# Kernel tuning notes

Hardware: AMD Instinct MI355X
Metric: run time of the kernel (lower is better)

The kernel has to match this reference:

```python
import jax, jax.numpy as jnp
import numpy as np
from jax import lax

D_MODEL = 128
D_INNER = 256   # expand * d_model
D_STATE = 16
D_CONV = 4
DT_RANK = 8     # ceil(d_model / 16)
IN_CH = 64
SCALE = 0.02


def setup_inputs() -> dict:
    key = jax.random.key(0)
    ks = jax.random.split(key, 16)
    r = lambda k, s: jax.random.normal(k, s, dtype=jnp.float32)
    return {
        "x": r(ks[0], (4, IN_CH, 128, 128)),
        "conv_w": r(ks[1], (D_MODEL, IN_CH, 3, 3)) * SCALE,
        "conv_b": r(ks[2], (D_MODEL,)) * SCALE,
        "bn_g": jnp.ones((D_MODEL,), jnp.float32),
        "bn_b": jnp.zeros((D_MODEL,), jnp.float32),
        "bn_mean": r(ks[3], (D_MODEL,)) * SCALE,
        "bn_var": jax.random.uniform(ks[4], (D_MODEL,), jnp.float32) + 0.5,
        "in_w": r(ks[5], (2 * D_INNER, D_MODEL)) * SCALE,
        "conv1d_w": r(ks[6], (D_INNER, 1, D_CONV)) * SCALE,
        "conv1d_b": r(ks[7], (D_INNER,)) * SCALE,
        "xproj_w": r(ks[8], (DT_RANK + 2 * D_STATE, D_INNER)) * SCALE,
        "dtproj_w": r(ks[9], (D_INNER, DT_RANK)) * SCALE,
        "dtproj_b": r(ks[10], (D_INNER,)) * SCALE,
        "A_log": r(ks[11], (D_INNER, D_STATE)) * 0.5,
        "Dp": r(ks[12], (D_INNER,)) * SCALE,
        "out_w": r(ks[13], (D_MODEL, D_INNER)) * SCALE,
    }


def _mamba(u, in_w, conv1d_w, conv1d_b, xproj_w, dtproj_w, dtproj_b, A_log, Dp, out_w):
    # u: [B, L, d_model]
    xz = jnp.einsum("bld,ed->ble", u, in_w)          # [B, L, 2*d_inner]
    x_in, z = jnp.split(xz, 2, axis=-1)
    # depthwise causal conv1d over L
    xc = lax.conv_general_dilated(
        x_in.transpose(0, 2, 1), conv1d_w, (1,), [(D_CONV - 1, 0)],
        dimension_numbers=("NCL", "OIL", "NCL"), feature_group_count=D_INNER,
    ) + conv1d_b[None, :, None]
    x_in = jax.nn.silu(xc).transpose(0, 2, 1)         # [B, L, d_inner]

    x_dbl = jnp.einsum("bld,ed->ble", x_in, xproj_w)  # [B, L, dt_rank+2*d_state]
    dt, Bm, Cm = jnp.split(x_dbl, [DT_RANK, DT_RANK + D_STATE], axis=-1)
    delta = jax.nn.softplus(jnp.einsum("blr,dr->bld", dt, dtproj_w) + dtproj_b)

    A = -jnp.exp(A_log)                               # [d_inner, d_state]
    deltaA = jnp.exp(jnp.einsum("bld,dn->bldn", delta, A))        # [B,L,d,n]
    deltaBu = jnp.einsum("bld,bln,bld->bldn", delta, Bm, x_in)    # [B,L,d,n]

    def step(h, inp):
        dA, dBu, c = inp                              # [B,d,n],[B,d,n],[B,n]
        h = dA * h + dBu
        y = jnp.einsum("bdn,bn->bd", h, c)
        return h, y

    Bsz, L = u.shape[0], u.shape[1]
    h0 = jnp.zeros((Bsz, D_INNER, D_STATE), u.dtype)
    _, ys = lax.scan(step, h0, (deltaA.transpose(1, 0, 2, 3),
                                deltaBu.transpose(1, 0, 2, 3),
                                Cm.transpose(1, 0, 2)))
    y = ys.transpose(1, 0, 2) + x_in * Dp             # [B, L, d_inner]
    y = y * jax.nn.silu(z)
    return jnp.einsum("bld,ed->ble", y, out_w)        # [B, L, d_model]


def reference(x, conv_w, conv_b, bn_g, bn_b, bn_mean, bn_var, in_w, conv1d_w,
              conv1d_b, xproj_w, dtproj_w, dtproj_b, A_log, Dp, out_w):
    # downsample: conv3x3 stride2 + BN(eval) + exact GELU
    y = lax.conv_general_dilated(x, conv_w, (2, 2), [(1, 1), (1, 1)],
                                 dimension_numbers=("NCHW", "OIHW", "NCHW"))
    y = y + conv_b[None, :, None, None]
    inv = bn_g / jnp.sqrt(bn_var + 1e-5)
    y = (y - bn_mean[None, :, None, None]) * inv[None, :, None, None] + bn_b[None, :, None, None]
    y = jax.nn.gelu(y, approximate=False)             # [B, C, H, W]

    B, C, H, W = y.shape
    u = y.reshape(B, C, H * W).transpose(0, 2, 1)     # [B, L, C]
    out = _mamba(u, in_w, conv1d_w, conv1d_b, xproj_w, dtproj_w, dtproj_b,
                 A_log, Dp, out_w)
    out = out.transpose(0, 2, 1).reshape(B, C, H, W)
    return y + out
```

## Files before the change

### kernel.cpp

```cpp
#include <hip/hip_runtime.h>
#include <math.h>

#define NB 4
#define LTOK 4096
#define DM 128
#define DI 256
#define NCH 256
#define TCH 16
#define GSZ 16
#define NG  16

#define OFF_A2     0u
#define OFF_BIAS2  73728u
#define OFF_YDSR   84096u
#define OFF_XPRE   2181248u
#define OFF_S0     4278400u
#define OFF_Z      6375552u
#define OFF_DELTA  10569856u
#define OFF_S1     12667008u
#define OFF_BC     14764160u
#define OFF_DSUM   15288448u
#define OFF_GS     15550592u
#define OFF_GD     15812736u
#define OFF_XT     15829120u
#define OFF_WBF    17926272u
#define OFF_WCMP   17963136u
#define OFF_YDSBF  18004096u
#define OFF_DPREF  18004096u
#define OFF_INWBF  19052672u
#define OFF_OUTWBF 19085440u

#define DEV __device__ __forceinline__
#define L2E 1.4426950408889634f

typedef short bh8 __attribute__((ext_vector_type(8)));
typedef float f4v __attribute__((ext_vector_type(4)));

DEV float fast_silu(float v) {
  return v * __builtin_amdgcn_rcpf(1.f + __expf(-v));
}

DEV unsigned short f2bf(float f) {
  unsigned int u = __float_as_uint(f);
  u = (u + 0x7FFFu + ((u >> 16) & 1u)) >> 16;
  return (unsigned short)u;
}

DEV float bf2f(unsigned short us) {
  return __uint_as_float((unsigned int)us << 16);
}

__global__ __launch_bounds__(256) void k0_prep(
    const float* __restrict__ conv_w, const float* __restrict__ conv_b,
    const float* __restrict__ bn_g, const float* __restrict__ bn_b,
    const float* __restrict__ bn_mean, const float* __restrict__ bn_var,
    const float* __restrict__ xproj_w, const float* __restrict__ A_log,
    const float* __restrict__ dtw, const float* __restrict__ in_w,
    const float* __restrict__ out_w, float* __restrict__ ws) {
  int i = blockIdx.x * 256 + threadIdx.x;
  if (i < 73728) {
    int ci = i & 63; int tap = (i >> 6) % 9; int co = i / 576;
    float inv = bn_g[co] * rsqrtf(bn_var[co] + 1e-5f);
    ((unsigned short*)(ws + OFF_WBF))[i] = f2bf(conv_w[co * 576 + ci * 9 + tap] * inv);
  } else if (i < 73856) {
    int co = i - 73728;
    float inv = bn_g[co] * rsqrtf(bn_var[co] + 1e-5f);
    ws[OFF_BIAS2 + co] = (conv_b[co] - bn_mean[co]) * inv + bn_b[co];
  } else if (i < 77952) {
    int j = i - 73856;
    ws[OFF_A2 + j] = -__expf(A_log[j]) * L2E;
  } else if (i < 159872) {
    int j = i - 77952;
    int n = j >> 8, k = j & 255;
    float v = 0.f;
    if (n < 256) {
#pragma unroll
      for (int r = 0; r < 8; ++r)
        v = fmaf(dtw[n * 8 + r], xproj_w[r * 256 + k], v);
    } else if (n < 288) {
      v = xproj_w[(8 + n - 256) * 256 + k];
    }
    ((unsigned short*)(ws + OFF_WCMP))[j] = f2bf(v);
  } else if (i < 225408) {
    int j = i - 159872;
    ((unsigned short*)(ws + OFF_INWBF))[j] = f2bf(in_w[j]);
  } else if (i < 258176) {
    int j = i - 225408;
    ((unsigned short*)(ws + OFF_OUTWBF))[j] = f2bf(out_w[j]);
  }
}

__global__ __launch_bounds__(256) void k0b_transpose(
    const float* __restrict__ x, unsigned short* __restrict__ xt) {
  __shared__ float t[64][65];
  const int tid = threadIdx.x;
  const int ixh = blockIdx.x & 1;
  const int iy = (blockIdx.x >> 1) & 127;
  const int b = blockIdx.x >> 8;
  {
    const int ixl = tid & 63, cw = tid >> 6;
#pragma unroll 4
    for (int i = 0; i < 16; ++i) {
      int ci = cw * 16 + i;
      t[ci][ixl] = x[(((size_t)(b * 64 + ci) * 128) + iy) * 128 + ixh * 64 + ixl];
    }
  }
  __syncthreads();
  {
    const int cil = tid & 63, iw = tid >> 6;
    unsigned short* dst = xt + (((size_t)(b * 128 + iy) * 128) + ixh * 64) * 64;
#pragma unroll 4
    for (int i = 0; i < 16; ++i) {
      int ix = iw * 16 + i;
      dst[ix * 64 + cil] = f2bf(t[cil][ix]);
    }
  }
}

__global__ __launch_bounds__(256) void k1_conv_mfma(
    const unsigned short* __restrict__ xt, const unsigned short* __restrict__ wbf,
    const float* __restrict__ bias2, unsigned short* __restrict__ ydsr,
    unsigned short* __restrict__ ydsbf) {
  __shared__ unsigned short ldt[64][66];
  const int tid = threadIdx.x;
  const int lane = tid & 63;
  const int w = tid >> 6;
  const int col = lane & 15, quad = lane >> 4;
  const int cohalf = blockIdx.x & 1;
  const int oy = (blockIdx.x >> 1) & 63;
  const int b = blockIdx.x >> 7;
  const int co0 = cohalf * 64 + (w & 1) * 32;
  const int tok0 = (w >> 1) * 32;
  const int iy0 = 2 * oy - 1;
  const bh8 bzero = {};
  f4v acc[2][2];
#pragma unroll
  for (int mt = 0; mt < 2; ++mt)
#pragma unroll
    for (int nt = 0; nt < 2; ++nt) acc[mt][nt] = (f4v){0.f, 0.f, 0.f, 0.f};

  const unsigned short* ap0 = wbf + (size_t)(co0 + col) * 576;
  const unsigned short* ap1 = wbf + (size_t)(co0 + 16 + col) * 576;

  for (int tap = 0; tap < 9; ++tap) {
    const int kh = tap / 3, kw = tap - kh * 3;
    const int iy = iy0 + kh;
    const int ix0 = 2 * (tok0 + col) - 1 + kw;
    const int ix1 = ix0 + 32;
    const unsigned short* xrow = xt + (long)(b * 128 + iy) * 8192;
    const bool ok0 = (iy >= 0) && (ix0 >= 0);
    const bool ok1 = (iy >= 0);
#pragma unroll
    for (int kc = 0; kc < 2; ++kc) {
      const int cib = kc * 32 + quad * 8;
      bh8 a0 = *(const bh8*)&ap0[tap * 64 + cib];
      bh8 a1 = *(const bh8*)&ap1[tap * 64 + cib];
      bh8 b0 = *(const bh8*)&xrow[(long)ix0 * 64 + cib];
      bh8 b1 = *(const bh8*)&xrow[(long)ix1 * 64 + cib];
      if (!ok0) b0 = bzero;
      if (!ok1) b1 = bzero;
      acc[0][0] = __builtin_amdgcn_mfma_f32_16x16x32_bf16(a0, b0, acc[0][0], 0, 0, 0);
      acc[1][0] = __builtin_amdgcn_mfma_f32_16x16x32_bf16(a1, b0, acc[1][0], 0, 0, 0);
      acc[0][1] = __builtin_amdgcn_mfma_f32_16x16x32_bf16(a0, b1, acc[0][1], 0, 0, 0);
      acc[1][1] = __builtin_amdgcn_mfma_f32_16x16x32_bf16(a1, b1, acc[1][1], 0, 0, 0);
    }
  }
#pragma unroll
  for (int mt = 0; mt < 2; ++mt)
#pragma unroll
    for (int nt = 0; nt < 2; ++nt) {
      const int tok = tok0 + nt * 16 + col;
#pragma unroll
      for (int r = 0; r < 4; ++r) {
        const int co = co0 + mt * 16 + quad * 4 + r;
        float v = acc[mt][nt][r] + bias2[co];
        float g = 0.5f * v * (1.f + erff(v * 0.70710678118f));
        unsigned short gb = f2bf(g);
        ydsr[(((size_t)(b * 128 + co) * 64) + oy) * 64 + tok] = gb;
        ldt[tok][(w & 1) * 32 + mt * 16 + quad * 4 + r] = gb;
      }
    }
  __syncthreads();
  {
    const int tok = tid >> 2, cg = (tid & 3) * 16;
    unsigned short* dst =
        ydsbf + ((size_t)(b * 4096 + oy * 64 + tok)) * 128 + cohalf * 64 + cg;
#pragma unroll
    for (int j = 0; j < 8; ++j)
      ((unsigned int*)dst)[j] = *(const unsigned int*)&ldt[tok][cg + 2 * j];
  }
}

__global__ __launch_bounds__(256) void k2_mfma(
    const unsigned short* __restrict__ ydsbf, const unsigned short* __restrict__ inwbf,
    unsigned short* __restrict__ xpre, unsigned short* __restrict__ z) {
  const int tid = threadIdx.x;
  const int lane = tid & 63;
  const int w = tid >> 6;
  const int col = lane & 15, quad = lane >> 4;
  const int tt = blockIdx.x & 255, b = blockIdx.x >> 8;
  const int t0 = tt * 16;
  bh8 afrag[4];
  {
    const unsigned short* arow = ydsbf + (size_t)(b * 4096 + t0 + col) * 128 + quad * 8;
#pragma unroll
    for (int kb = 0; kb < 4; ++kb) afrag[kb] = *(const bh8*)&arow[kb * 32];
  }
  f4v acc[8];
#pragma unroll
  for (int j = 0; j < 8; ++j) acc[j] = (f4v){0.f, 0.f, 0.f, 0.f};
  const int nt0 = w * 8;
  const unsigned short* wb = inwbf + (size_t)(nt0 * 16 + col) * 128 + quad * 8;
#pragma unroll
  for (int kb = 0; kb < 4; ++kb) {
#pragma unroll
    for (int j = 0; j < 8; ++j) {
      bh8 bfrag = *(const bh8*)&wb[(size_t)j * 2048 + kb * 32];
      acc[j] = __builtin_amdgcn_mfma_f32_16x16x32_bf16(afrag[kb], bfrag, acc[j], 0, 0, 0);
    }
  }
#pragma unroll
  for (int j = 0; j < 8; ++j) {
    const int e = (nt0 + j) * 16 + col;
#pragma unroll
    for (int r = 0; r < 4; ++r) {
      const int t = t0 + quad * 4 + r;
      if (e < 256) xpre[((size_t)(b * 4096 + t)) * 256 + e] = f2bf(acc[j][r]);
      else z[((size_t)(b * 4096 + t)) * 256 + e - 256] = f2bf(acc[j][r]);
    }
  }
}

__global__ __launch_bounds__(256) void k45_mfma(
    const unsigned short* __restrict__ wcomp, const float* __restrict__ dtb,
    const unsigned short* __restrict__ xpre, const float* __restrict__ cw1,
    const float* __restrict__ cb1, const float* __restrict__ a2tab,
    unsigned short* __restrict__ xinbf, unsigned short* __restrict__ delta,
    float* __restrict__ bc, float* __restrict__ dsum,
    float* __restrict__ S0, float* __restrict__ S1) {
  __shared__ unsigned short ld_xin[16][264];
  __shared__ unsigned short ld_delta[16][264];
  __shared__ float ld_bc[16][33];
  const int tid = threadIdx.x;
  const int lane = tid & 63;
  const int w = tid >> 6;
  const int col = lane & 15, quad = lane >> 4;
  const int tt = blockIdx.x & 255, b = blockIdx.x >> 8;
  const int t0 = tt * 16;

  {
    const int d = tid;
    float4 w4 = *(const float4*)&cw1[d * 4];
    float bias = cb1[d];
    float xw[19];
#pragma unroll
    for (int i = 0; i < 19; ++i) {
      int t = t0 - 3 + i;
      xw[i] = (t >= 0) ? bf2f(xpre[((size_t)(b * 4096 + t)) * 256 + d]) : 0.f;
    }
    unsigned short* dst = xinbf + ((size_t)(b * 4096 + t0)) * 256 + d;
#pragma unroll
    for (int i = 0; i < 16; ++i) {
      float o = bias + w4.x * xw[i] + w4.y * xw[i + 1] + w4.z * xw[i + 2] +
                w4.w * xw[i + 3];
      unsigned short us = f2bf(fast_silu(o));
      ld_xin[i][d] = us;
      dst[(size_t)i * 256] = us;
    }
  }
  __syncthreads();

  {
    bh8 afrag[8];
#pragma unroll
    for (int kb = 0; kb < 8; ++kb)
      afrag[kb] = *(const bh8*)&ld_xin[col][quad * 8 + kb * 32];
    f4v acc[5];
#pragma unroll
    for (int j = 0; j < 5; ++j) acc[j] = (f4v){0.f, 0.f, 0.f, 0.f};

    const int nt0 = w * 5;
    const unsigned short* wb = wcomp + (size_t)(nt0 * 16 + col) * 256 + quad * 8;
#pragma unroll
    for (int kb = 0; kb < 8; ++kb) {
#pragma unroll
      for (int j = 0; j < 5; ++j) {
        bh8 bfrag = *(const bh8*)&wb[(size_t)j * 4096 + kb * 32];
        acc[j] = __builtin_amdgcn_mfma_f32_16x16x32_bf16(afrag[kb], bfrag, acc[j], 0, 0, 0);
      }
    }
#pragma unroll
    for (int j = 0; j < 5; ++j) {
      const int n = (nt0 + j) * 16 + col;
      if (n < 256) {
        float bias = dtb[n];
#pragma unroll
        for (int r = 0; r < 4; ++r) {
          float s = acc[j][r] + bias;
          float dl = fmaxf(s, 0.f) + __logf(1.f + __expf(-fabsf(s)));
          ld_delta[quad * 4 + r][n] = f2bf(dl);
        }
      } else if (n < 288) {
#pragma unroll
        for (int r = 0; r < 4; ++r) ld_bc[quad * 4 + r][n - 256] = acc[j][r];
      }
    }
  }
  __syncthreads();

  {
    const int d = tid;
    float A2[16];
#pragma unroll
    for (int j = 0; j < 4; ++j) {
      float4 a = *(const float4*)&a2tab[d * 16 + j * 4];
      A2[4 * j + 0] = a.x; A2[4 * j + 1] = a.y;
      A2[4 * j + 2] = a.z; A2[4 * j + 3] = a.w;
    }
    float h[16];
#pragma unroll
    for (int n = 0; n < 16; ++n) h[n] = 0.f;
    float ds = 0.f;
#pragma unroll 4
    for (int i = 0; i < TCH; ++i) {
      float dl = bf2f(ld_delta[i][d]);
      float xv = bf2f(ld_xin[i][d]);
      ds += dl;
      float dlx = dl * xv;
#pragma unroll
      for (int n = 0; n < 16; ++n)
        h[n] = fmaf(exp2f(dl * A2[n]), h[n], dlx * ld_bc[i][n]);
    }
    dsum[((size_t)b * NCH + tt) * 256 + d] = ds;
    float* S = (b & 2) ? (S1 + (size_t)(b & 1) * 1048576)
                       : (S0 + (size_t)(b & 1) * 1048576);
    const size_t sbase = ((size_t)tt * 16) * 256 + d;
#pragma unroll
    for (int n = 0; n < 16; ++n) S[sbase + (size_t)n * 256] = h[n];
  }

#pragma unroll
  for (int it = 0; it < 4; ++it) {
    int idx = it * 256 + tid;
    int row = idx >> 6, d4 = (idx & 63) * 4;
    unsigned long long pk = *(const unsigned long long*)&ld_delta[row][d4];
    *(unsigned long long*)&delta[((size_t)(b * 4096 + t0 + row)) * 256 + d4] = pk;
  }
  if (tid < 128) {
    int row = tid >> 3, q = (tid & 7) * 4;
    float4 v = make_float4(ld_bc[row][q], ld_bc[row][q + 1],
                           ld_bc[row][q + 2], ld_bc[row][q + 3]);
    *(float4*)&bc[((size_t)(b * 4096 + t0 + row)) * 32 + q] = v;
  }
}

__global__ __launch_bounds__(256) void k5b1_group(
    float* __restrict__ S0, float* __restrict__ S1,
    const float* __restrict__ dsum, const float* __restrict__ a2tab,
    float* __restrict__ Gs, float* __restrict__ Gd,
    float* __restrict__ dpref) {
  const int d = threadIdx.x;
  const int n = blockIdx.x & 15, g = (blockIdx.x >> 4) & (NG - 1),
            b = blockIdx.x >> 8;
  float* S = (b & 2) ? (S1 + (size_t)(b & 1) * 1048576)
                     : (S0 + (size_t)(b & 1) * 1048576);
  const float A2 = a2tab[d * 16 + n];
  const size_t s0 = ((size_t)(g * GSZ) * 16 + n) * 256 + d;
  const size_t d0 = ((size_t)b * NCH + g * GSZ) * 256 + d;
  float sv[GSZ], dv[GSZ];
#pragma unroll
  for (int k = 0; k < GSZ; ++k) {
    sv[k] = S[s0 + (size_t)k * 4096];
    dv[k] = dsum[d0 + (size_t)k * 256];
  }
  float h = 0.f, cum = 0.f;
#pragma unroll
  for (int k = 0; k < GSZ; ++k) {
    S[s0 + (size_t)k * 4096] = h;
    if (n == 0) dpref[d0 + (size_t)k * 256] = cum;
    h = fmaf(exp2f(A2 * dv[k]), h, sv[k]);
    cum += dv[k];
  }
  Gs[((size_t)(b * NG + g) * 16 + n) * 256 + d] = h;
  if (n == 0) Gd[((size_t)b * NG + g) * 256 + d] = cum;
}

__global__ __launch_bounds__(256) void k5b2_groupscan(
    float* __restrict__ Gs, const float* __restrict__ Gd,
    const float* __restrict__ a2tab) {
  const int d = threadIdx.x;
  const int n = blockIdx.x & 15, b = blockIdx.x >> 4;
  const float A2 = a2tab[d * 16 + n];
  float sv[NG], dv[NG];
  const size_t g0 = ((size_t)(b * NG) * 16 + n) * 256 + d;
  const size_t gd0 = (size_t)b * NG * 256 + d;
#pragma unroll
  for (int g = 0; g < NG; ++g) {
    sv[g] = Gs[g0 + (size_t)g * 4096];
    dv[g] = Gd[gd0 + (size_t)g * 256];
  }
  float h = 0.f;
#pragma unroll
  for (int g = 0; g < NG; ++g) {
    Gs[g0 + (size_t)g * 4096] = h;
    h = fmaf(exp2f(A2 * dv[g]), h, sv[g]);
  }
}

__global__ __launch_bounds__(256) void k56_fused(
    const unsigned short* __restrict__ xinbf, const float* __restrict__ bc,
    const unsigned short* __restrict__ delta, const unsigned short* __restrict__ z,
    const float* __restrict__ a2tab, const float* __restrict__ Dp,
    const float* __restrict__ dpref, const float* __restrict__ Gs,
    const float* __restrict__ S0, const float* __restrict__ S1,
    const unsigned short* __restrict__ outwbf, const unsigned short* __restrict__ ydsr,
    float* __restrict__ out) {
  __shared__ __align__(16) float bct[TCH * 32];
  __shared__ __align__(16) unsigned short ld_y[16][264];
  __shared__ float ldo[16][132];
  const int tid = threadIdx.x;
  const int d = tid;
  const int c = blockIdx.x & (NCH - 1), b = blockIdx.x >> 8;
  const int t0 = c * TCH;
  {
    const float* src = bc + (size_t)(b * 4096 + t0) * 32;
    for (int i = tid; i < TCH * 32; i += 256) bct[i] = src[i];
  }
  float A2[16];
#pragma unroll
  for (int j = 0; j < 4; ++j) {
    float4 a = *(const float4*)&a2tab[d * 16 + j * 4];
    A2[4 * j + 0] = a.x; A2[4 * j + 1] = a.y;
    A2[4 * j + 2] = a.z; A2[4 * j + 3] = a.w;
  }
  const float Dpd = Dp[d];
  const int g = c >> 4;
  const float dp0 = dpref[((size_t)b * NCH + c) * 256 + d];
  const float* S = (b & 2) ? (S1 + (size_t)(b & 1) * 1048576)
                           : (S0 + (size_t)(b & 1) * 1048576);
  const size_t sbase = ((size_t)c * 16) * 256 + d;
  const size_t gbase = ((size_t)(b * NG + g) * 16) * 256 + d;
  float h[16];
#pragma unroll
  for (int n = 0; n < 16; ++n) {
    float gi = Gs[gbase + (size_t)n * 256];
    float hl = S[sbase + (size_t)n * 256];
    h[n] = fmaf(exp2f(A2[n] * dp0), gi, hl);
  }
  const size_t base = (size_t)(b * 4096 + t0) * 256 + d;
  const unsigned short* pd = delta + base;
  const unsigned short* px = xinbf + base;
  const unsigned short* pz = z + base;
  __syncthreads();
#pragma unroll 4
  for (int i = 0; i < TCH; ++i) {
    float dl = bf2f(pd[(size_t)i * 256]);
    float xv = bf2f(px[(size_t)i * 256]);
    float zv = bf2f(pz[(size_t)i * 256]);
    float dlx = dl * xv;
    const float* r = &bct[i * 32];
    float4 B0 = *(const float4*)&r[0];
    float4 B1 = *(const float4*)&r[4];
    float4 B2 = *(const float4*)&r[8];
    float4 B3 = *(const float4*)&r[12];
    float4 C0 = *(const float4*)&r[16];
    float4 C1 = *(const float4*)&r[20];
    float4 C2 = *(const float4*)&r[24];
    float4 C3 = *(const float4*)&r[28];
    float Bv[16] = {B0.x, B0.y, B0.z, B0.w, B1.x, B1.y, B1.z, B1.w,
                    B2.x, B2.y, B2.z, B2.w, B3.x, B3.y, B3.z, B3.w};
    float Cv[16] = {C0.x, C0.y, C0.z, C0.w, C1.x, C1.y, C1.z, C1.w,
                    C2.x, C2.y, C2.z, C2.w, C3.x, C3.y, C3.z, C3.w};
    float y = 0.f;
#pragma unroll
    for (int n = 0; n < 16; ++n) {
      h[n] = fmaf(exp2f(dl * A2[n]), h[n], dlx * Bv[n]);
      y = fmaf(h[n], Cv[n], y);
    }
    ld_y[i][d] = f2bf((y + xv * Dpd) * fast_silu(zv));
  }
  __syncthreads();

  const int lane = tid & 63;
  const int w = tid >> 6;
  const int col = lane & 15, quad = lane >> 4;
  const int oy = t0 >> 6, ox0 = t0 & 63;
  bh8 afrag[8];
#pragma unroll
  for (int kb = 0; kb < 8; ++kb)
    afrag[kb] = *(const bh8*)&ld_y[col][quad * 8 + kb * 32];
  f4v acc[2];
#pragma unroll
  for (int j = 0; j < 2; ++j) acc[j] = (f4v){0.f, 0.f, 0.f, 0.f};
  const int nt0 = w * 2;
  const unsigned short* wb = outwbf + (size_t)(nt0 * 16 + col) * 256 + quad * 8;
#pragma unroll
  for (int kb = 0; kb < 8; ++kb) {
#pragma unroll
    for (int j = 0; j < 2; ++j) {
      bh8 bfrag = *(const bh8*)&wb[(size_t)j * 4096 + kb * 32];
      acc[j] = __builtin_amdgcn_mfma_f32_16x16x32_bf16(afrag[kb], bfrag, acc[j], 0, 0, 0);
    }
  }
#pragma unroll
  for (int j = 0; j < 2; ++j)
#pragma unroll
    for (int r = 0; r < 4; ++r)
      ldo[quad * 4 + r][(nt0 + j) * 16 + col] = acc[j][r];
  __syncthreads();
  {
    const int cc = tid >> 1, half = tid & 1;
    size_t obase = (((size_t)(b * 128 + cc) * 64) + oy) * 64 + ox0 + half * 8;
    const unsigned short* rp = ydsr + obase;
    const int m0 = half * 8;
    float4 o0 = make_float4(ldo[m0 + 0][cc] + bf2f(rp[0]), ldo[m0 + 1][cc] + bf2f(rp[1]),
                            ldo[m0 + 2][cc] + bf2f(rp[2]), ldo[m0 + 3][cc] + bf2f(rp[3]));
    float4 o1 = make_float4(ldo[m0 + 4][cc] + bf2f(rp[4]), ldo[m0 + 5][cc] + bf2f(rp[5]),
                            ldo[m0 + 6][cc] + bf2f(rp[6]), ldo[m0 + 7][cc] + bf2f(rp[7]));
    *(float4*)&out[obase] = o0;
    *(float4*)&out[obase + 4] = o1;
  }
}

extern "C" void kernel_launch(void* const* d_in, const int* in_sizes, int n_in,
                              void* d_out, int out_size, void* d_ws, size_t ws_size,
                              hipStream_t stream) {
  (void)in_sizes; (void)n_in; (void)out_size; (void)ws_size;
  const float* x        = (const float*)d_in[0];
  const float* conv_w   = (const float*)d_in[1];
  const float* conv_b   = (const float*)d_in[2];
  const float* bn_g     = (const float*)d_in[3];
  const float* bn_b     = (const float*)d_in[4];
  const float* bn_mean  = (const float*)d_in[5];
  const float* bn_var   = (const float*)d_in[6];
  const float* in_w     = (const float*)d_in[7];
  const float* conv1d_w = (const float*)d_in[8];
  const float* conv1d_b = (const float*)d_in[9];
  const float* xproj_w  = (const float*)d_in[10];
  const float* dtproj_w = (const float*)d_in[11];
  const float* dtproj_b = (const float*)d_in[12];
  const float* A_log    = (const float*)d_in[13];
  const float* Dp       = (const float*)d_in[14];
  const float* out_w    = (const float*)d_in[15];
  float* ws = (float*)d_ws;
  float* out = (float*)d_out;

  k0_prep<<<1009, 256, 0, stream>>>(conv_w, conv_b, bn_g, bn_b, bn_mean, bn_var,
                                    xproj_w, A_log, dtproj_w, in_w, out_w, ws);
  k0b_transpose<<<1024, 256, 0, stream>>>(x, (unsigned short*)(ws + OFF_XT));
  k1_conv_mfma<<<512, 256, 0, stream>>>((const unsigned short*)(ws + OFF_XT),
                                        (const unsigned short*)(ws + OFF_WBF),
                                        ws + OFF_BIAS2,
                                        (unsigned short*)(ws + OFF_YDSR),
                                        (unsigned short*)(ws + OFF_YDSBF));
  k2_mfma<<<1024, 256, 0, stream>>>((const unsigned short*)(ws + OFF_YDSBF),
                                    (const unsigned short*)(ws + OFF_INWBF),
                                    (unsigned short*)(ws + OFF_XPRE),
                                    (unsigned short*)(ws + OFF_Z));
  k45_mfma<<<1024, 256, 0, stream>>>((const unsigned short*)(ws + OFF_WCMP),
                                     dtproj_b,
                                     (const unsigned short*)(ws + OFF_XPRE),
                                     conv1d_w, conv1d_b, ws + OFF_A2,
                                     (unsigned short*)(ws + OFF_XT),
                                     (unsigned short*)(ws + OFF_DELTA),
                                     ws + OFF_BC, ws + OFF_DSUM,
                                     ws + OFF_S0, ws + OFF_S1);
  k5b1_group<<<1024, 256, 0, stream>>>(ws + OFF_S0, ws + OFF_S1, ws + OFF_DSUM,
                                       ws + OFF_A2, ws + OFF_GS, ws + OFF_GD,
                                       ws + OFF_DPREF);
  k5b2_groupscan<<<64, 256, 0, stream>>>(ws + OFF_GS, ws + OFF_GD, ws + OFF_A2);
  k56_fused<<<1024, 256, 0, stream>>>((const unsigned short*)(ws + OFF_XT),
                                      ws + OFF_BC,
                                      (const unsigned short*)(ws + OFF_DELTA),
                                      (const unsigned short*)(ws + OFF_Z),
                                      ws + OFF_A2, Dp, ws + OFF_DPREF,
                                      ws + OFF_GS, ws + OFF_S0, ws + OFF_S1,
                                      (const unsigned short*)(ws + OFF_OUTWBF),
                                      (const unsigned short*)(ws + OFF_YDSR), out);
}
```

Baseline: 215.7 us.

## Fuse conv with in-projection, merge prep with transpose, and inline group scan

Merges the weight-prep and input-transpose kernels into one launch using a block-index split. Fuses the 3x3 conv+GELU kernel with the in-projection GEMM so each block keeps its 64 tokens x 128 channels tile in swizzled LDS. This removes the ydsbf round trip through global memory. Drops the separate group-scan kernel; each k56 block now recomputes the prefix over earlier groups from Gs/Gd. That adds redundant serial work (up to 15 steps) and fewer, larger conv blocks (256 blocks of 512 threads).

```diff
diff --git a/kernel.cpp b/kernel.cpp
--- a/kernel.cpp
+++ b/kernel.cpp
@@ -25,7 +25,6 @@
 #define OFF_XT     15829120u
 #define OFF_WBF    17926272u
 #define OFF_WCMP   17963136u
-#define OFF_YDSBF  18004096u
 #define OFF_DPREF  18004096u
 #define OFF_INWBF  19052672u
 #define OFF_OUTWBF 19085440u
@@ -50,13 +49,42 @@
   return __uint_as_float((unsigned int)us << 16);
 }
 
-__global__ __launch_bounds__(256) void k0_prep(
+__global__ __launch_bounds__(256) void k0x_prep(
     const float* __restrict__ conv_w, const float* __restrict__ conv_b,
     const float* __restrict__ bn_g, const float* __restrict__ bn_b,
     const float* __restrict__ bn_mean, const float* __restrict__ bn_var,
     const float* __restrict__ xproj_w, const float* __restrict__ A_log,
     const float* __restrict__ dtw, const float* __restrict__ in_w,
-    const float* __restrict__ out_w, float* __restrict__ ws) {
+    const float* __restrict__ out_w, const float* __restrict__ x,
+    float* __restrict__ ws) {
+  __shared__ float t[64][65];
+  if (blockIdx.x >= 1009) {
+    const int bid = blockIdx.x - 1009;
+    unsigned short* xt = (unsigned short*)(ws + OFF_XT);
+    const int tid = threadIdx.x;
+    const int ixh = bid & 1;
+    const int iy = (bid >> 1) & 127;
+    const int b = bid >> 8;
+    {
+      const int ixl = tid & 63, cw = tid >> 6;
+#pragma unroll 4
+      for (int i = 0; i < 16; ++i) {
+        int ci = cw * 16 + i;
+        t[ci][ixl] = x[(((size_t)(b * 64 + ci) * 128) + iy) * 128 + ixh * 64 + ixl];
+      }
+    }
+    __syncthreads();
+    {
+      const int cil = tid & 63, iw = tid >> 6;
+      unsigned short* dst = xt + (((size_t)(b * 128 + iy) * 128) + ixh * 64) * 64;
+#pragma unroll 4
+      for (int i = 0; i < 16; ++i) {
+        int ix = iw * 16 + i;
+        dst[ix * 64 + cil] = f2bf(t[cil][ix]);
+      }
+    }
+    return;
+  }
   int i = blockIdx.x * 256 + threadIdx.x;
   if (i < 73728) {
     int ci = i & 63; int tap = (i >> 6) % 9; int co = i / 576;
@@ -90,143 +118,90 @@
   }
 }
 
-__global__ __launch_bounds__(256) void k0b_transpose(
-    const float* __restrict__ x, unsigned short* __restrict__ xt) {
-  __shared__ float t[64][65];
-  const int tid = threadIdx.x;
-  const int ixh = blockIdx.x & 1;
-  const int iy = (blockIdx.x >> 1) & 127;
-  const int b = blockIdx.x >> 8;
-  {
-    const int ixl = tid & 63, cw = tid >> 6;
-#pragma unroll 4
-    for (int i = 0; i < 16; ++i) {
-      int ci = cw * 16 + i;
-      t[ci][ixl] = x[(((size_t)(b * 64 + ci) * 128) + iy) * 128 + ixh * 64 + ixl];
-    }
-  }
-  __syncthreads();
-  {
-    const int cil = tid & 63, iw = tid >> 6;
-    unsigned short* dst = xt + (((size_t)(b * 128 + iy) * 128) + ixh * 64) * 64;
-#pragma unroll 4
-    for (int i = 0; i < 16; ++i) {
-      int ix = iw * 16 + i;
-      dst[ix * 64 + cil] = f2bf(t[cil][ix]);
-    }
-  }
-}
-
-__global__ __launch_bounds__(256) void k1_conv_mfma(
+__global__ __launch_bounds__(512) void k12_conv_inproj(
     const unsigned short* __restrict__ xt, const unsigned short* __restrict__ wbf,
-    const float* __restrict__ bias2, unsigned short* __restrict__ ydsr,
-    unsigned short* __restrict__ ydsbf) {
-  __shared__ unsigned short ldt[64][66];
+    const float* __restrict__ bias2, const unsigned short* __restrict__ inwbf,
+    unsigned short* __restrict__ ydsr, unsigned short* __restrict__ xpre,
+    unsigned short* __restrict__ z) {
+  __shared__ unsigned short ldt[64][136];
   const int tid = threadIdx.x;
   const int lane = tid & 63;
   const int w = tid >> 6;
   const int col = lane & 15, quad = lane >> 4;
-  const int cohalf = blockIdx.x & 1;
-  const int oy = (blockIdx.x >> 1) & 63;
-  const int b = blockIdx.x >> 7;
-  const int co0 = cohalf * 64 + (w & 1) * 32;
-  const int tok0 = (w >> 1) * 32;
+  const int oy = blockIdx.x & 63;
+  const int b = blockIdx.x >> 6;
+  const int co_w = w * 16;
   const int iy0 = 2 * oy - 1;
   const bh8 bzero = {};
-  f4v acc[2][2];
-#pragma unroll
-  for (int mt = 0; mt < 2; ++mt)
-#pragma unroll
-    for (int nt = 0; nt < 2; ++nt) acc[mt][nt] = (f4v){0.f, 0.f, 0.f, 0.f};
-
-  const unsigned short* ap0 = wbf + (size_t)(co0 + col) * 576;
-  const unsigned short* ap1 = wbf + (size_t)(co0 + 16 + col) * 576;
-
+
+  f4v acc[4];
+#pragma unroll
+  for (int nt = 0; nt < 4; ++nt) acc[nt] = (f4v){0.f, 0.f, 0.f, 0.f};
+  const unsigned short* ap = wbf + (size_t)(co_w + col) * 576;
   for (int tap = 0; tap < 9; ++tap) {
     const int kh = tap / 3, kw = tap - kh * 3;
     const int iy = iy0 + kh;
-    const int ix0 = 2 * (tok0 + col) - 1 + kw;
-    const int ix1 = ix0 + 32;
     const unsigned short* xrow = xt + (long)(b * 128 + iy) * 8192;
-    const bool ok0 = (iy >= 0) && (ix0 >= 0);
-    const bool ok1 = (iy >= 0);
+    const bool oky = (iy >= 0);
 #pragma unroll
     for (int kc = 0; kc < 2; ++kc) {
       const int cib = kc * 32 + quad * 8;
-      bh8 a0 = *(const bh8*)&ap0[tap * 64 + cib];
-      bh8 a1 = *(const bh8*)&ap1[tap * 64 + cib];
-      bh8 b0 = *(const bh8*)&xrow[(long)ix0 * 64 + cib];
-      bh8 b1 = *(const bh8*)&xrow[(long)ix1 * 64 + cib];
-      if (!ok0) b0 = bzero;
-      if (!ok1) b1 = bzero;
-      acc[0][0] = __builtin_amdgcn_mfma_f32_16x16x32_bf16(a0, b0, acc[0][0], 0, 0, 0);
-      acc[1][0] = __builtin_amdgcn_mfma_f32_16x16x32_bf16(a1, b0, acc[1][0], 0, 0, 0);
-      acc[0][1] = __builtin_amdgcn_mfma_f32_16x16x32_bf16(a0, b1, acc[0][1], 0, 0, 0);
-      acc[1][1] = __builtin_amdgcn_mfma_f32_16x16x32_bf16(a1, b1, acc[1][1], 0, 0, 0);
-    }
-  }
-#pragma unroll
-  for (int mt = 0; mt < 2; ++mt)
-#pragma unroll
-    for (int nt = 0; nt < 2; ++nt) {
-      const int tok = tok0 + nt * 16 + col;
+      bh8 a0 = *(const bh8*)&ap[tap * 64 + cib];
+#pragma unroll
+      for (int nt = 0; nt < 4; ++nt) {
+        const int ix = 2 * (nt * 16 + col) - 1 + kw;
+        bh8 bv = *(const bh8*)&xrow[(long)ix * 64 + cib];
+        if (!(oky && ix >= 0)) bv = bzero;
+        acc[nt] = __builtin_amdgcn_mfma_f32_16x16x32_bf16(a0, bv, acc[nt], 0, 0, 0);
+      }
+    }
+  }
+#pragma unroll
+  for (int nt = 0; nt < 4; ++nt) {
+    const int tok = nt * 16 + col;
+    const int swz = (tok & 15) << 3;
+#pragma unroll
+    for (int r = 0; r < 4; ++r) {
+      const int co = co_w + quad * 4 + r;
+      float v = acc[nt][r] + bias2[co];
+      float g = 0.5f * v * (1.f + erff(v * 0.70710678118f));
+      unsigned short gb = f2bf(g);
+      ydsr[(((size_t)(b * 128 + co) * 64) + oy) * 64 + tok] = gb;
+      ldt[tok][co ^ swz] = gb;
+    }
+  }
+  __syncthreads();
+
+  const size_t tglob0 = (size_t)(b * 4096 + oy * 64);
+#pragma unroll
+  for (int tt = 0; tt < 4; ++tt) {
+    const int row = tt * 16 + col;
+    const int swz = (row & 15) << 3;
+    bh8 afrag[4];
+#pragma unroll
+    for (int kb = 0; kb < 4; ++kb)
+      afrag[kb] = *(const bh8*)&ldt[row][(quad * 8 + kb * 32) ^ swz];
+    f4v acc2[4];
+#pragma unroll
+    for (int j = 0; j < 4; ++j) acc2[j] = (f4v){0.f, 0.f, 0.f, 0.f};
+#pragma unroll
+    for (int kb = 0; kb < 4; ++kb) {
+#pragma unroll
+      for (int j = 0; j < 4; ++j) {
+        const int e_row = (w * 4 + j) * 16 + col;
+        bh8 bfrag = *(const bh8*)&inwbf[(size_t)e_row * 128 + quad * 8 + kb * 32];
+        acc2[j] = __builtin_amdgcn_mfma_f32_16x16x32_bf16(afrag[kb], bfrag, acc2[j], 0, 0, 0);
+      }
+    }
+#pragma unroll
+    for (int j = 0; j < 4; ++j) {
+      const int e = (w * 4 + j) * 16 + col;
 #pragma unroll
       for (int r = 0; r < 4; ++r) {
-        const int co = co0 + mt * 16 + quad * 4 + r;
-        float v = acc[mt][nt][r] + bias2[co];
-        float g = 0.5f * v * (1.f + erff(v * 0.70710678118f));
-        unsigned short gb = f2bf(g);
-        ydsr[(((size_t)(b * 128 + co) * 64) + oy) * 64 + tok] = gb;
-        ldt[tok][(w & 1) * 32 + mt * 16 + quad * 4 + r] = gb;
-      }
-    }
-  __syncthreads();
-  {
-    const int tok = tid >> 2, cg = (tid & 3) * 16;
-    unsigned short* dst =
-        ydsbf + ((size_t)(b * 4096 + oy * 64 + tok)) * 128 + cohalf * 64 + cg;
-#pragma unroll
-    for (int j = 0; j < 8; ++j)
-      ((unsigned int*)dst)[j] = *(const unsigned int*)&ldt[tok][cg + 2 * j];
-  }
-}
-
-__global__ __launch_bounds__(256) void k2_mfma(
-    const unsigned short* __restrict__ ydsbf, const unsigned short* __restrict__ inwbf,
-    unsigned short* __restrict__ xpre, unsigned short* __restrict__ z) {
-  const int tid = threadIdx.x;
-  const int lane = tid & 63;
-  const int w = tid >> 6;
-  const int col = lane & 15, quad = lane >> 4;
-  const int tt = blockIdx.x & 255, b = blockIdx.x >> 8;
-  const int t0 = tt * 16;
-  bh8 afrag[4];
-  {
-    const unsigned short* arow = ydsbf + (size_t)(b * 4096 + t0 + col) * 128 + quad * 8;
-#pragma unroll
-    for (int kb = 0; kb < 4; ++kb) afrag[kb] = *(const bh8*)&arow[kb * 32];
-  }
-  f4v acc[8];
-#pragma unroll
-  for (int j = 0; j < 8; ++j) acc[j] = (f4v){0.f, 0.f, 0.f, 0.f};
-  const int nt0 = w * 8;
-  const unsigned short* wb = inwbf + (size_t)(nt0 * 16 + col) * 128 + quad * 8;
-#pragma unroll
-  for (int kb = 0; kb < 4; ++kb) {
-#pragma unroll
-    for (int j = 0; j < 8; ++j) {
-      bh8 bfrag = *(const bh8*)&wb[(size_t)j * 2048 + kb * 32];
-      acc[j] = __builtin_amdgcn_mfma_f32_16x16x32_bf16(afrag[kb], bfrag, acc[j], 0, 0, 0);
-    }
-  }
-#pragma unroll
-  for (int j = 0; j < 8; ++j) {
-    const int e = (nt0 + j) * 16 + col;
-#pragma unroll
-    for (int r = 0; r < 4; ++r) {
-      const int t = t0 + quad * 4 + r;
-      if (e < 256) xpre[((size_t)(b * 4096 + t)) * 256 + e] = f2bf(acc[j][r]);
-      else z[((size_t)(b * 4096 + t)) * 256 + e - 256] = f2bf(acc[j][r]);
+        const size_t t = tglob0 + tt * 16 + quad * 4 + r;
+        if (e < 256) xpre[t * 256 + e] = f2bf(acc2[j][r]);
+        else z[t * 256 + e - 256] = f2bf(acc2[j][r]);
+      }
     }
   }
 }
@@ -385,33 +360,12 @@
   if (n == 0) Gd[((size_t)b * NG + g) * 256 + d] = cum;
 }
 
-__global__ __launch_bounds__(256) void k5b2_groupscan(
-    float* __restrict__ Gs, const float* __restrict__ Gd,
-    const float* __restrict__ a2tab) {
-  const int d = threadIdx.x;
-  const int n = blockIdx.x & 15, b = blockIdx.x >> 4;
-  const float A2 = a2tab[d * 16 + n];
-  float sv[NG], dv[NG];
-  const size_t g0 = ((size_t)(b * NG) * 16 + n) * 256 + d;
-  const size_t gd0 = (size_t)b * NG * 256 + d;
-#pragma unroll
-  for (int g = 0; g < NG; ++g) {
-    sv[g] = Gs[g0 + (size_t)g * 4096];
-    dv[g] = Gd[gd0 + (size_t)g * 256];
-  }
-  float h = 0.f;
-#pragma unroll
-  for (int g = 0; g < NG; ++g) {
-    Gs[g0 + (size_t)g * 4096] = h;
-    h = fmaf(exp2f(A2 * dv[g]), h, sv[g]);
-  }
-}
-
 __global__ __launch_bounds__(256) void k56_fused(
     const unsigned short* __restrict__ xinbf, const float* __restrict__ bc,
     const unsigned short* __restrict__ delta, const unsigned short* __restrict__ z,
     const float* __restrict__ a2tab, const float* __restrict__ Dp,
     const float* __restrict__ dpref, const float* __restrict__ Gs,
+    const float* __restrict__ Gd,
     const float* __restrict__ S0, const float* __restrict__ S1,
     const unsigned short* __restrict__ outwbf, const unsigned short* __restrict__ ydsr,
     float* __restrict__ out) {
@@ -439,13 +393,20 @@
   const float* S = (b & 2) ? (S1 + (size_t)(b & 1) * 1048576)
                            : (S0 + (size_t)(b & 1) * 1048576);
   const size_t sbase = ((size_t)c * 16) * 256 + d;
-  const size_t gbase = ((size_t)(b * NG + g) * 16) * 256 + d;
   float h[16];
 #pragma unroll
+  for (int n = 0; n < 16; ++n) h[n] = 0.f;
+  for (int gp = 0; gp < g; ++gp) {
+    const float gdv = Gd[((size_t)b * NG + gp) * 256 + d];
+    const size_t gb0 = ((size_t)(b * NG + gp) * 16) * 256 + d;
+#pragma unroll
+    for (int n = 0; n < 16; ++n)
+      h[n] = fmaf(exp2f(A2[n] * gdv), h[n], Gs[gb0 + (size_t)n * 256]);
+  }
+#pragma unroll
   for (int n = 0; n < 16; ++n) {
-    float gi = Gs[gbase + (size_t)n * 256];
     float hl = S[sbase + (size_t)n * 256];
-    h[n] = fmaf(exp2f(A2[n] * dp0), gi, hl);
+    h[n] = fmaf(exp2f(A2[n] * dp0), h[n], hl);
   }
   const size_t base = (size_t)(b * 4096 + t0) * 256 + d;
   const unsigned short* pd = delta + base;
@@ -545,18 +506,15 @@
   float* ws = (float*)d_ws;
   float* out = (float*)d_out;
 
-  k0_prep<<<1009, 256, 0, stream>>>(conv_w, conv_b, bn_g, bn_b, bn_mean, bn_var,
-                                    xproj_w, A_log, dtproj_w, in_w, out_w, ws);
-  k0b_transpose<<<1024, 256, 0, stream>>>(x, (unsigned short*)(ws + OFF_XT));
-  k1_conv_mfma<<<512, 256, 0, stream>>>((const unsigned short*)(ws + OFF_XT),
-                                        (const unsigned short*)(ws + OFF_WBF),
-                                        ws + OFF_BIAS2,
-                                        (unsigned short*)(ws + OFF_YDSR),
-                                        (unsigned short*)(ws + OFF_YDSBF));
-  k2_mfma<<<1024, 256, 0, stream>>>((const unsigned short*)(ws + OFF_YDSBF),
-                                    (const unsigned short*)(ws + OFF_INWBF),
-                                    (unsigned short*)(ws + OFF_XPRE),
-                                    (unsigned short*)(ws + OFF_Z));
+  k0x_prep<<<2033, 256, 0, stream>>>(conv_w, conv_b, bn_g, bn_b, bn_mean, bn_var,
+                                     xproj_w, A_log, dtproj_w, in_w, out_w, x, ws);
+  k12_conv_inproj<<<256, 512, 0, stream>>>(
+      (const unsigned short*)(ws + OFF_XT),
+      (const unsigned short*)(ws + OFF_WBF), ws + OFF_BIAS2,
+      (const unsigned short*)(ws + OFF_INWBF),
+      (unsigned short*)(ws + OFF_YDSR),
+      (unsigned short*)(ws + OFF_XPRE),
+      (unsigned short*)(ws + OFF_Z));
   k45_mfma<<<1024, 256, 0, stream>>>((const unsigned short*)(ws + OFF_WCMP),
                                      dtproj_b,
                                      (const unsigned short*)(ws + OFF_XPRE),
@@ -568,13 +526,13 @@
   k5b1_group<<<1024, 256, 0, stream>>>(ws + OFF_S0, ws + OFF_S1, ws + OFF_DSUM,
                                        ws + OFF_A2, ws + OFF_GS, ws + OFF_GD,
                                        ws + OFF_DPREF);
-  k5b2_groupscan<<<64, 256, 0, stream>>>(ws + OFF_GS, ws + OFF_GD, ws + OFF_A2);
   k56_fused<<<1024, 256, 0, stream>>>((const unsigned short*)(ws + OFF_XT),
                                       ws + OFF_BC,
                                       (const unsigned short*)(ws + OFF_DELTA),
                                       (const unsigned short*)(ws + OFF_Z),
                                       ws + OFF_A2, Dp, ws + OFF_DPREF,
-                                      ws + OFF_GS, ws + OFF_S0, ws + OFF_S1,
+                                      ws + OFF_GS, ws + OFF_GD,
+                                      ws + OFF_S0, ws + OFF_S1,
                                       (const unsigned short*)(ws + OFF_OUTWBF),
                                       (const unsigned short*)(ws + OFF_YDSR), out);
 }
```

Result: no change. 216.2 us (+0.2%).
